# Performance work log

Measured on AMD Instinct MI355X. Metric: run time of the kernel, lower is better.

Reference implementation:

```python
import math
import jax, jax.numpy as jnp
import numpy as np

B, S, HID, NH = 8, 512, 1024, 16
D = HID // NH          # head dim = 64
SPAN = 512             # att_span = max_relative_positions = max_position_embeddings


def _linear(x, W, b):
    # torch nn.Linear: y = x @ W.T + b, W is [out, in]
    return jnp.einsum('...i,oi->...o', x, W) + b


def _heads(x):
    # [B, S, HID] -> [B, NH, S, D]
    b, s, _ = x.shape
    return x.reshape(b, s, NH, D).transpose(0, 2, 1, 3)


def setup_inputs() -> dict:
    key = jax.random.key(0)
    ks = jax.random.split(key, 16)
    f = lambda i, shape, sc=1.0: jax.random.normal(ks[i], shape, dtype=jnp.float32) * sc
    return {
        'q': f(0, (B, S, HID)),
        'k': f(1, (B, S, HID)),
        'v': f(2, (B, S, HID)),
        'attention_mask': jnp.tril(jnp.ones((S, S), dtype=bool))[None, None],  # causal [1,1,S,S]
        'Wq': f(3, (HID, HID), 0.02), 'bq': jnp.zeros((HID,), jnp.float32),
        'Wk': f(4, (HID, HID), 0.02), 'bk': jnp.zeros((HID,), jnp.float32),
        'Wv': f(5, (HID, HID), 0.02), 'bv': jnp.zeros((HID,), jnp.float32),
        'Wpk': f(6, (HID, HID), 0.02), 'bpk': jnp.zeros((HID,), jnp.float32),
        'Wpq': f(7, (HID, HID), 0.02), 'bpq': jnp.zeros((HID,), jnp.float32),
        'rel_emb': f(8, (2 * SPAN, HID), 0.02),
    }


def reference(q, k, v, attention_mask, Wq, bq, Wk, bk, Wv, bv, Wpk, bpk, Wpq, bpq, rel_emb):
    scale_factor = 3  # 1 (content) + c2p + p2c
    scale = 1.0 / math.sqrt(D * scale_factor)

    ql = _heads(_linear(q, Wq, bq))   # [B,NH,S,D]
    kl = _heads(_linear(k, Wk, bk))
    vl = _heads(_linear(v, Wv, bv))

    # content-to-content scores
    scores = jnp.einsum('bhqd,bhkd->bhqk', ql, kl) * scale

    # relative positions (no bucketing since position_buckets = -1)
    rel = jnp.arange(S)[:, None] - jnp.arange(S)[None, :]          # [S,S]
    c2p_pos = jnp.clip(rel + SPAN, 0, 2 * SPAN - 1)
    p2c_pos = jnp.clip(-rel + SPAN, 0, 2 * SPAN - 1)

    # projected relative-position embeddings -> [NH, 2*SPAN, D]
    pk = _linear(rel_emb, Wpk, bpk).reshape(2 * SPAN, NH, D).transpose(1, 0, 2)
    pq = _linear(rel_emb, Wpq, bpq).reshape(2 * SPAN, NH, D).transpose(1, 0, 2)

    # content-to-position: out[b,h,q,k] = (q . pos_key)[b,h,q, c2p_pos[q,k]]
    c2p = jnp.einsum('bhqd,hjd->bhqj', ql, pk) * scale             # [B,NH,S,2*SPAN]
    c2p = jnp.take_along_axis(c2p, jnp.broadcast_to(c2p_pos[None, None], (B, NH, S, S)), axis=-1)

    # position-to-content: gathered[b,h,k,q] = (k . pos_query)[b,h,k, p2c_pos[k,q]], then transpose
    p2c = jnp.einsum('bhkd,hjd->bhkj', kl, pq) * scale             # [B,NH,S,2*SPAN]
    p2c = jnp.take_along_axis(p2c, jnp.broadcast_to(p2c_pos[None, None], (B, NH, S, S)), axis=-1)

    scores = scores + c2p + jnp.swapaxes(p2c, -1, -2)
    # subtract detached row max (as in torch: .max(...).values.detach())
    scores = scores - jax.lax.stop_gradient(scores.max(axis=-1, keepdims=True))

    # XSoftmax: masked softmax, then zero masked positions
    neg = jnp.float32(-1e30)
    probs = jax.nn.softmax(jnp.where(attention_mask, scores, neg), axis=-1)
    probs = jnp.where(attention_mask, probs, 0.0)

    ctx = jnp.einsum('bhqk,bhkd->bhqd', probs, vl)                 # [B,NH,S,D]
    return ctx.transpose(0, 2, 1, 3).reshape(B, S, HID)
```

## Files before the change

kernel.cpp:

```cpp
#include <hip/hip_runtime.h>
#include <hip/hip_bf16.h>
#include <math.h>

#define SCALE 0.07216878364870323f
#define NEG_BIG -1e30f

typedef __attribute__((ext_vector_type(8))) short bf16x8;
typedef __attribute__((ext_vector_type(4))) short bf16x4;
typedef __attribute__((ext_vector_type(4))) float f32x4;
#define MFMA_BF16 __builtin_amdgcn_mfma_f32_16x16x32_bf16

#define BARX()   asm volatile("s_barrier" ::: "memory")
#define VMCNT0() asm volatile("s_waitcnt vmcnt(0)" ::: "memory")
#define LGKM0()  do { asm volatile("s_waitcnt lgkmcnt(0)" ::: "memory"); \
                      __builtin_amdgcn_sched_barrier(0); } while (0)

static __device__ __forceinline__ float bf2f(__hip_bfloat16 x) { return __bfloat162float(x); }
static __device__ __forceinline__ __hip_bfloat16 f2bf(float x) { return __float2bfloat16(x); }
static __device__ __forceinline__ short f2bs(float x) {
  union { __hip_bfloat16 b; short s; } u; u.b = __float2bfloat16(x); return u.s;
}
static __device__ __forceinline__ float s2f(short v) {
  union { float f; unsigned u; } x; x.u = ((unsigned)(unsigned short)v) << 16; return x.f;
}
static __device__ __forceinline__ bf16x4 cvt4(float4 f) {
  bf16x4 r; r[0] = f2bs(f.x); r[1] = f2bs(f.y); r[2] = f2bs(f.z); r[3] = f2bs(f.w);
  return r;
}
static __device__ __forceinline__ bf16x8 ldg8(const __hip_bfloat16* p) {
  return *(const bf16x8*)p;
}
static __device__ __forceinline__ void gl_lds16(const __hip_bfloat16* g, __hip_bfloat16* l) {
  __builtin_amdgcn_global_load_lds(
      (const __attribute__((address_space(1))) void*)g,
      (__attribute__((address_space(3))) void*)l, 16, 0, 0);
}

struct CvtJob { const float* src; __hip_bfloat16* dst; int n4; };
struct CvtArgs { CvtJob j[9]; };

__global__ __launch_bounds__(256) void cvt_kernel(CvtArgs a) {
  const CvtJob jb = a.j[blockIdx.y];
  const float4* s = (const float4*)jb.src;
  bf16x4* d = (bf16x4*)jb.dst;
  const int stride = gridDim.x * 256;
  for (int i = blockIdx.x * 256 + threadIdx.x; i < jb.n4; i += stride)
    d[i] = cvt4(s[i]);
}

struct Gemm { const __hip_bfloat16* A; const __hip_bfloat16* W;
              const float* bias; __hip_bfloat16* out; int mode; int mBits; int nBlk;
              float oscale; };
struct ProjArgs { Gemm g[5]; };

static __device__ __forceinline__ void stage_half(const __hip_bfloat16* gtile,
                                                  __hip_bfloat16* ltile,
                                                  int half, int wave, int lane) {
  const int r = lane >> 3;
  const int chunk = (lane & 7) ^ r;
#pragma unroll
  for (int c = 0; c < 2; c++) {
    const int rowbase = half * 128 + c * 64 + wave * 8;
    gl_lds16(gtile + (size_t)(rowbase + r) * 1024 + chunk * 8,
             ltile + (size_t)rowbase * 64);
  }
}

__global__ __launch_bounds__(512, 2) void proj_kernel(ProjArgs pa) {
  const Gemm g = pa.g[blockIdx.y];
  if ((int)blockIdx.x >= g.nBlk) return;
  __shared__ __hip_bfloat16 As[2][256][64];
  __shared__ __hip_bfloat16 Ws[2][256][64];

  const int bid = blockIdx.x;
  const int m0 = (bid & ((1 << g.mBits) - 1)) * 256;
  const int n0 = (bid >> g.mBits) * 256;
  const int tid = threadIdx.x;
  const int wave = tid >> 6, lane = tid & 63;
  const int q16 = lane >> 4, l16 = lane & 15;
  const int wr = wave >> 2, wc = wave & 3;
  const int l7 = l16 & 7;

  const __hip_bfloat16* Ag = g.A + (size_t)m0 * 1024;
  const __hip_bfloat16* Wg = g.W + (size_t)n0 * 1024;

  f32x4 acc[8][4] = {};

  stage_half(Ag, &As[0][0][0], 0, wave, lane);
  stage_half(Ag, &As[0][0][0], 1, wave, lane);
  stage_half(Wg, &Ws[0][0][0], 0, wave, lane);
  stage_half(Wg, &Ws[0][0][0], 1, wave, lane);
  VMCNT0();
  BARX();

  for (int t = 0; t < 16; ++t) {
    const int sl = t & 1, sn = sl ^ 1;
    const __hip_bfloat16* Ac = &As[sl][0][0];
    const __hip_bfloat16* Wc = &Ws[sl][0][0];
    const bool pf = (t + 1 < 16);
    const __hip_bfloat16* gA1 = Ag + (size_t)(t + 1) * 64;
    const __hip_bfloat16* gW1 = Wg + (size_t)(t + 1) * 64;

    bf16x8 bw[4], af[4];
#pragma unroll
    for (int kh = 0; kh < 2; kh++) {
      const int csw = ((kh * 4 + q16) ^ l7) * 8;

#pragma unroll
      for (int ni = 0; ni < 4; ni++)
        bw[ni] = *(const bf16x8*)(Wc + (size_t)(wc * 64 + ni * 16 + l16) * 64 + csw);
#pragma unroll
      for (int mi = 0; mi < 4; mi++)
        af[mi] = *(const bf16x8*)(Ac + (size_t)(wr * 128 + mi * 16 + l16) * 64 + csw);
      if (pf) {
        if (kh == 0) stage_half(gA1, &As[sn][0][0], 0, wave, lane);
        else         stage_half(gW1, &Ws[sn][0][0], 0, wave, lane);
      }
      BARX();
      LGKM0();
      __builtin_amdgcn_s_setprio(1);
#pragma unroll
      for (int ni = 0; ni < 4; ni++)
#pragma unroll
        for (int mi = 0; mi < 4; mi++)
          acc[mi][ni] = MFMA_BF16(af[mi], bw[ni], acc[mi][ni], 0, 0, 0);
      __builtin_amdgcn_s_setprio(0);
      BARX();

#pragma unroll
      for (int mi = 0; mi < 4; mi++)
        af[mi] = *(const bf16x8*)(Ac + (size_t)(wr * 128 + 64 + mi * 16 + l16) * 64 + csw);
      if (pf) {
        if (kh == 0) stage_half(gA1, &As[sn][0][0], 1, wave, lane);
        else         stage_half(gW1, &Ws[sn][0][0], 1, wave, lane);
      }
      BARX();
      LGKM0();
      __builtin_amdgcn_s_setprio(1);
#pragma unroll
      for (int ni = 0; ni < 4; ni++)
#pragma unroll
        for (int mi = 0; mi < 4; mi++)
          acc[4 + mi][ni] = MFMA_BF16(af[mi], bw[ni], acc[4 + mi][ni], 0, 0, 0);
      __builtin_amdgcn_s_setprio(0);
      if (kh == 1 && pf) VMCNT0();
      BARX();
    }
  }

#pragma unroll
  for (int ni = 0; ni < 4; ni++) {
    const int n = n0 + wc * 64 + ni * 16 + l16;
#pragma unroll
    for (int mi = 0; mi < 8; mi++) {
#pragma unroll
      for (int rr = 0; rr < 4; rr++) {
        const int m = m0 + wr * 128 + mi * 16 + q16 * 4 + rr;
        float val = acc[mi][ni][rr];
        size_t oidx;
        if (g.mode == 0) {
          val = (val + g.bias[n]) * g.oscale;
          const int b = m >> 9, s = m & 511;
          const int h = n >> 6, d = n & 63;
          oidx = ((size_t)((b * 16 + h) * 512 + s)) * 64 + d;
        } else if (g.mode == 1) {
          val = (val + g.bias[m]) * g.oscale;
          const int b = n >> 9, s = n & 511;
          const int h = m >> 6, d = m & 63;
          oidx = ((size_t)((b * 16 + h) * 64 + d)) * 512 + s;
        } else {
          val = (val + g.bias[n]) * g.oscale;
          const int h = n >> 6, d = n & 63;
          oidx = ((size_t)(h * 512 + m)) * 64 + d;
        }
        g.out[oidx] = f2bf(val);
      }
    }
  }
}

__global__ __launch_bounds__(256) void attn_kernel(
    const __hip_bfloat16* __restrict__ ql,
    const __hip_bfloat16* __restrict__ kl,
    const __hip_bfloat16* __restrict__ vlT,
    const __hip_bfloat16* __restrict__ pk,
    const __hip_bfloat16* __restrict__ pq,
    float* __restrict__ out)
{
  __shared__ __align__(16) __hip_bfloat16 pool[2][64][72];
  __shared__ __align__(16) __hip_bfloat16 pqs[2][32][72];
  __shared__ __align__(16) float qkbuf[32][36];
  __shared__ __align__(16) __hip_bfloat16 cpb[2][32][68];
  __shared__ __align__(16) __hip_bfloat16 pT[64][36];
  __shared__ __align__(16) __hip_bfloat16 ptile[32][40];
  __shared__ __align__(16) __hip_bfloat16 vt[64][40];
  __shared__ float mred[32];
  __shared__ float rsum[32];

  const int bid = blockIdx.x;
  const int qt = 15 - (bid >> 7);
  const int bh = bid & 127;
  const int h = bh & 15, b = bh >> 4;
  const int q0 = qt * 32;

  const __hip_bfloat16* qlp = ql + (size_t)bh * 512 * 64;
  const __hip_bfloat16* klp = kl + (size_t)bh * 512 * 64;
  const __hip_bfloat16* vtp = vlT + (size_t)bh * 64 * 512;
  const __hip_bfloat16* pkp = pk + (size_t)h * 512 * 64;
  const __hip_bfloat16* pqp = pq + (size_t)h * 512 * 64;

  const int tid = threadIdx.x, wave = tid >> 6, lane = tid & 63;
  const int q16 = lane >> 4, l16 = lane & 15;
  const int wr = wave & 1, wc = wave >> 1;

  bf16x8 qlB[2][2];
#pragma unroll
  for (int ksi = 0; ksi < 2; ksi++)
#pragma unroll
    for (int bq = 0; bq < 2; bq++)
      qlB[ksi][bq] = ldg8(qlp + (size_t)(q0 + bq * 16 + l16) * 64 + ksi * 32 + q16 * 8);

  {
    int4 z = {0, 0, 0, 0};
    *(int4*)(&pqs[1][tid >> 3][(tid & 7) * 8]) = z;
  }

  const int kEnd = q0 + 32;
  const int nIter = kEnd >> 5;

  const int sr = tid >> 3, sseg = tid & 7;
  const int vr = tid >> 2, vs = tid & 3;
  int4 rKv, rPKv, rPQv, rVt;
  {
    rKv  = ((const int4*)(klp + (size_t)(q0 + sr) * 64))[sseg];
    rPKv = ((const int4*)(pkp + (size_t)(0 + sr) * 64))[sseg];
    rPQv = ((const int4*)(pqp + (size_t)(0 + sr) * 64))[sseg];
    rVt  = ((const int4*)(vtp + (size_t)vr * 512 + q0))[vs];
  }

  const int aq = tid >> 3;
  const int kb = (tid & 7) * 4;
  float m_old = -INFINITY, s_part = 0.f;
  f32x4 octx[2] = {};

  for (int it = 0; it < nIter; ++it) {
    const int k0 = q0 - it * 32;
    const int par = it & 1;
    *(int4*)(&pool[par][sr][sseg * 8])      = rKv;
    *(int4*)(&pool[par][32 + sr][sseg * 8]) = rPKv;
    *(int4*)(&pqs[par][sr][sseg * 8])       = rPQv;
    if (it + 1 < nIter) {
      const int k0n = k0 - 32, jbn = (it + 1) * 32;
      rKv  = ((const int4*)(klp + (size_t)(k0n + sr) * 64))[sseg];
      rPKv = ((const int4*)(pkp + (size_t)(jbn + sr) * 64))[sseg];
      rPQv = ((const int4*)(pqp + (size_t)(jbn + sr) * 64))[sseg];
    }
    __syncthreads();

    const int arb = (wave == 1) ? 32 : 0;
    f32x4 a4[2][2] = {};
    __builtin_amdgcn_s_setprio(1);
#pragma unroll
    for (int ksi = 0; ksi < 2; ksi++) {
      const int ko = ksi * 32 + q16 * 8;
      bf16x8 Af0 = *(const bf16x8*)(&pool[par][arb + l16][ko]);
      bf16x8 Af1 = *(const bf16x8*)(&pool[par][arb + 16 + l16][ko]);
      bf16x8 Bf0, Bf1;
      if (wave < 2) {
        Bf0 = qlB[ksi][0];
        Bf1 = qlB[ksi][1];
      } else {
        const int ps = (wave == 2) ? (par ^ 1) : par;
        Bf0 = *(const bf16x8*)(&pqs[ps][l16][ko]);
        Bf1 = *(const bf16x8*)(&pqs[ps][16 + l16][ko]);
      }
      a4[0][0] = MFMA_BF16(Af0, Bf0, a4[0][0], 0, 0, 0);
      a4[0][1] = MFMA_BF16(Af0, Bf1, a4[0][1], 0, 0, 0);
      a4[1][0] = MFMA_BF16(Af1, Bf0, a4[1][0], 0, 0, 0);
      a4[1][1] = MFMA_BF16(Af1, Bf1, a4[1][1], 0, 0, 0);
    }
    __builtin_amdgcn_s_setprio(0);
    if (wave == 0) {
#pragma unroll
      for (int a = 0; a < 2; a++)
#pragma unroll
        for (int bq = 0; bq < 2; bq++)
          *(f32x4*)(&qkbuf[bq * 16 + l16][a * 16 + q16 * 4]) = a4[a][bq];
    } else if (wave == 1) {
#pragma unroll
      for (int a = 0; a < 2; a++)
#pragma unroll
        for (int bq = 0; bq < 2; bq++) {
          bf16x4 v;
#pragma unroll
          for (int r = 0; r < 4; r++) v[r] = f2bs(a4[a][bq][r]);
          const int q = bq * 16 + l16, jr = a * 16 + q16 * 4;
          *(bf16x4*)(&cpb[par][q][32 + jr]) = v;
          *(bf16x4*)(&cpb[par ^ 1][q][jr]) = v;
        }
    } else {
      const int rb = (wave == 3) ? 32 : 0;
#pragma unroll
      for (int a = 0; a < 2; a++)
#pragma unroll
        for (int bq = 0; bq < 2; bq++) {
          bf16x4 v;
#pragma unroll
          for (int r = 0; r < 4; r++) v[r] = f2bs(a4[a][bq][r]);
          *(bf16x4*)(&pT[rb + bq * 16 + l16][a * 16 + q16 * 4]) = v;
        }
    }
    __syncthreads();

    {
      const f32x4 qk4 = *(const f32x4*)(&qkbuf[aq][kb]);
      float v[4];
      float tmax = -INFINITY;
#pragma unroll
      for (int j = 0; j < 4; j++) {
        const int dlt = aq - (kb + j);
        v[j] = qk4[j] + bf2f(cpb[par][aq][dlt + 32]) + bf2f(pT[dlt + 32][kb + j]);
        if ((it == 0) && (dlt < 0)) v[j] = -INFINITY;
        else tmax = fmaxf(tmax, v[j]);
      }
      tmax = fmaxf(tmax, __shfl_xor(tmax, 1));
      tmax = fmaxf(tmax, __shfl_xor(tmax, 2));
      tmax = fmaxf(tmax, __shfl_xor(tmax, 4));
      const float m_new = fmaxf(m_old, tmax);
      const float f = __expf(m_old - m_new);
      bf16x4 pv4;
      float psum = 0.f;
#pragma unroll
      for (int j = 0; j < 4; j++) {
        const float p = __expf(v[j] - m_new);
        pv4[j] = f2bs(p);
        psum += p;
      }
      s_part = s_part * f + psum;
      m_old = m_new;
      *(bf16x4*)(&ptile[aq][kb]) = pv4;
      if ((tid & 7) == 0) mred[aq] = f;
    }
    {
      *(int4*)(&vt[vr][vs * 8]) = rVt;
      if (it + 1 < nIter)
        rVt = ((const int4*)(vtp + (size_t)vr * 512 + (k0 - 32)))[vs];
    }
    __syncthreads();

    {
      float fr[4];
#pragma unroll
      for (int rr = 0; rr < 4; rr++) fr[rr] = mred[wr * 16 + q16 * 4 + rr];
      bf16x8 af = *(const bf16x8*)(&ptile[wr * 16 + l16][q16 * 8]);
      __builtin_amdgcn_s_setprio(1);
#pragma unroll
      for (int cs = 0; cs < 2; cs++) {
        bf16x8 bv = *(const bf16x8*)(&vt[wc * 32 + cs * 16 + l16][q16 * 8]);
        f32x4 c = octx[cs];
#pragma unroll
        for (int rr = 0; rr < 4; rr++) c[rr] *= fr[rr];
        octx[cs] = MFMA_BF16(af, bv, c, 0, 0, 0);
      }
      __builtin_amdgcn_s_setprio(0);
    }
  }

  {
    float s = s_part;
    s += __shfl_xor(s, 1);
    s += __shfl_xor(s, 2);
    s += __shfl_xor(s, 4);
    if ((tid & 7) == 0) rsum[aq] = s;
  }
  __syncthreads();

  for (int cs = 0; cs < 2; cs++) {
    const int d = wc * 32 + cs * 16 + l16;
    for (int rr = 0; rr < 4; rr++) {
      const int qh = wr * 16 + q16 * 4 + rr;
      const float val = octx[cs][rr] / rsum[qh];
      out[((size_t)(b * 512 + q0 + qh)) * 1024 + h * 64 + d] = val;
    }
  }
}

extern "C" void kernel_launch(void* const* d_in, const int* in_sizes, int n_in,
                              void* d_out, int out_size, void* d_ws, size_t ws_size,
                              hipStream_t stream) {
  const float* q   = (const float*)d_in[0];
  const float* k   = (const float*)d_in[1];
  const float* v   = (const float*)d_in[2];
  const float* Wq  = (const float*)d_in[4];
  const float* bq  = (const float*)d_in[5];
  const float* Wk  = (const float*)d_in[6];
  const float* bk  = (const float*)d_in[7];
  const float* Wv  = (const float*)d_in[8];
  const float* bv  = (const float*)d_in[9];
  const float* Wpk = (const float*)d_in[10];
  const float* bpk = (const float*)d_in[11];
  const float* Wpq = (const float*)d_in[12];
  const float* bpq = (const float*)d_in[13];
  const float* rel = (const float*)d_in[14];
  float* out = (float*)d_out;

  char* ws = (char*)d_ws;
  const size_t MB = 1u << 20;
  __hip_bfloat16* bqi  = (__hip_bfloat16*)(ws);
  __hip_bfloat16* bki  = (__hip_bfloat16*)(ws + 8 * MB);
  __hip_bfloat16* bvi  = (__hip_bfloat16*)(ws + 16 * MB);
  __hip_bfloat16* bWq  = (__hip_bfloat16*)(ws + 24 * MB);
  __hip_bfloat16* bWk  = (__hip_bfloat16*)(ws + 26 * MB);
  __hip_bfloat16* bWv  = (__hip_bfloat16*)(ws + 28 * MB);
  __hip_bfloat16* bWpk = (__hip_bfloat16*)(ws + 30 * MB);
  __hip_bfloat16* bWpq = (__hip_bfloat16*)(ws + 32 * MB);
  __hip_bfloat16* brel = (__hip_bfloat16*)(ws + 34 * MB);
  __hip_bfloat16* wql  = (__hip_bfloat16*)(ws + 35 * MB);
  __hip_bfloat16* wkl  = (__hip_bfloat16*)(ws + 43 * MB);
  __hip_bfloat16* wvlT = (__hip_bfloat16*)(ws + 51 * MB);
  __hip_bfloat16* wpk  = (__hip_bfloat16*)(ws + 59 * MB);
  __hip_bfloat16* wpq  = (__hip_bfloat16*)(ws + 60 * MB);

  CvtArgs ca;
  ca.j[0] = { q,   bqi,  4194304 / 4 };
  ca.j[1] = { k,   bki,  4194304 / 4 };
  ca.j[2] = { v,   bvi,  4194304 / 4 };
  ca.j[3] = { Wq,  bWq,  1048576 / 4 };
  ca.j[4] = { Wk,  bWk,  1048576 / 4 };
  ca.j[5] = { Wv,  bWv,  1048576 / 4 };
  ca.j[6] = { Wpk, bWpk, 1048576 / 4 };
  ca.j[7] = { Wpq, bWpq, 1048576 / 4 };
  ca.j[8] = { rel + (size_t)512 * 1024, brel, 524288 / 4 };
  cvt_kernel<<<dim3(1024, 9), 256, 0, stream>>>(ca);

  ProjArgs pj;
  pj.g[0] = { bqi,  bWq,  bq,  wql,  0, 4, 64, SCALE };
  pj.g[1] = { bki,  bWk,  bk,  wkl,  0, 4, 64, 1.0f };
  pj.g[2] = { bWv,  bvi,  bv,  wvlT, 1, 2, 64, 1.0f };
  pj.g[3] = { brel, bWpk, bpk, wpk,  2, 1, 8,  1.0f };
  pj.g[4] = { brel, bWpq, bpq, wpq,  2, 1, 8,  SCALE };
  proj_kernel<<<dim3(64, 5), 512, 0, stream>>>(pj);

  attn_kernel<<<2048, 256, 0, stream>>>(wql, wkl, wvlT, wpk, wpq, out);
}
```

Baseline: 231.4 us.

## Shrink projection GEMM tile to 256x128 and drop double-buffered LDS pipeline

```diff
diff --git a/kernel.cpp b/kernel.cpp
--- a/kernel.cpp
+++ b/kernel.cpp
@@ -9,11 +9,6 @@
 typedef __attribute__((ext_vector_type(4))) short bf16x4;
 typedef __attribute__((ext_vector_type(4))) float f32x4;
 #define MFMA_BF16 __builtin_amdgcn_mfma_f32_16x16x32_bf16
-
-#define BARX()   asm volatile("s_barrier" ::: "memory")
-#define VMCNT0() asm volatile("s_waitcnt vmcnt(0)" ::: "memory")
-#define LGKM0()  do { asm volatile("s_waitcnt lgkmcnt(0)" ::: "memory"); \
-                      __builtin_amdgcn_sched_barrier(0); } while (0)
 
 static __device__ __forceinline__ float bf2f(__hip_bfloat16 x) { return __bfloat162float(x); }
 static __device__ __forceinline__ __hip_bfloat16 f2bf(float x) { return __float2bfloat16(x); }
@@ -53,14 +48,15 @@
               float oscale; };
 struct ProjArgs { Gemm g[5]; };
 
-static __device__ __forceinline__ void stage_half(const __hip_bfloat16* gtile,
+static __device__ __forceinline__ void stage_tile(const __hip_bfloat16* gtile,
                                                   __hip_bfloat16* ltile,
-                                                  int half, int wave, int lane) {
+                                                  int nrows, int wave, int lane) {
   const int r = lane >> 3;
   const int chunk = (lane & 7) ^ r;
 #pragma unroll
-  for (int c = 0; c < 2; c++) {
-    const int rowbase = half * 128 + c * 64 + wave * 8;
+  for (int c = 0; c < 4; c++) {
+    if (c * 64 >= nrows) break;
+    const int rowbase = c * 64 + wave * 8;
     gl_lds16(gtile + (size_t)(rowbase + r) * 1024 + chunk * 8,
              ltile + (size_t)rowbase * 64);
   }
@@ -69,55 +65,38 @@
 __global__ __launch_bounds__(512, 2) void proj_kernel(ProjArgs pa) {
   const Gemm g = pa.g[blockIdx.y];
   if ((int)blockIdx.x >= g.nBlk) return;
-  __shared__ __hip_bfloat16 As[2][256][64];
-  __shared__ __hip_bfloat16 Ws[2][256][64];
+  __shared__ __hip_bfloat16 As[256][64];
+  __shared__ __hip_bfloat16 Ws[128][64];
 
   const int bid = blockIdx.x;
   const int m0 = (bid & ((1 << g.mBits) - 1)) * 256;
-  const int n0 = (bid >> g.mBits) * 256;
+  const int n0 = (bid >> g.mBits) * 128;
   const int tid = threadIdx.x;
   const int wave = tid >> 6, lane = tid & 63;
   const int q16 = lane >> 4, l16 = lane & 15;
-  const int wr = wave >> 2, wc = wave & 3;
+  const int wr = wave >> 1, wc = wave & 1;
   const int l7 = l16 & 7;
 
   const __hip_bfloat16* Ag = g.A + (size_t)m0 * 1024;
   const __hip_bfloat16* Wg = g.W + (size_t)n0 * 1024;
 
-  f32x4 acc[8][4] = {};
-
-  stage_half(Ag, &As[0][0][0], 0, wave, lane);
-  stage_half(Ag, &As[0][0][0], 1, wave, lane);
-  stage_half(Wg, &Ws[0][0][0], 0, wave, lane);
-  stage_half(Wg, &Ws[0][0][0], 1, wave, lane);
-  VMCNT0();
-  BARX();
+  f32x4 acc[4][4] = {};
 
   for (int t = 0; t < 16; ++t) {
-    const int sl = t & 1, sn = sl ^ 1;
-    const __hip_bfloat16* Ac = &As[sl][0][0];
-    const __hip_bfloat16* Wc = &Ws[sl][0][0];
-    const bool pf = (t + 1 < 16);
-    const __hip_bfloat16* gA1 = Ag + (size_t)(t + 1) * 64;
-    const __hip_bfloat16* gW1 = Wg + (size_t)(t + 1) * 64;
-
-    bf16x8 bw[4], af[4];
+    __syncthreads();
+    stage_tile(Ag + t * 64, &As[0][0], 256, wave, lane);
+    stage_tile(Wg + t * 64, &Ws[0][0], 128, wave, lane);
+    __syncthreads();
 #pragma unroll
     for (int kh = 0; kh < 2; kh++) {
       const int csw = ((kh * 4 + q16) ^ l7) * 8;
-
+      bf16x8 bw[4], af[4];
 #pragma unroll
       for (int ni = 0; ni < 4; ni++)
-        bw[ni] = *(const bf16x8*)(Wc + (size_t)(wc * 64 + ni * 16 + l16) * 64 + csw);
+        bw[ni] = *(const bf16x8*)(&Ws[wc * 64 + ni * 16 + l16][0] + csw);
 #pragma unroll
       for (int mi = 0; mi < 4; mi++)
-        af[mi] = *(const bf16x8*)(Ac + (size_t)(wr * 128 + mi * 16 + l16) * 64 + csw);
-      if (pf) {
-        if (kh == 0) stage_half(gA1, &As[sn][0][0], 0, wave, lane);
-        else         stage_half(gW1, &Ws[sn][0][0], 0, wave, lane);
-      }
-      BARX();
-      LGKM0();
+        af[mi] = *(const bf16x8*)(&As[wr * 64 + mi * 16 + l16][0] + csw);
       __builtin_amdgcn_s_setprio(1);
 #pragma unroll
       for (int ni = 0; ni < 4; ni++)
@@ -125,26 +104,6 @@
         for (int mi = 0; mi < 4; mi++)
           acc[mi][ni] = MFMA_BF16(af[mi], bw[ni], acc[mi][ni], 0, 0, 0);
       __builtin_amdgcn_s_setprio(0);
-      BARX();
-
-#pragma unroll
-      for (int mi = 0; mi < 4; mi++)
-        af[mi] = *(const bf16x8*)(Ac + (size_t)(wr * 128 + 64 + mi * 16 + l16) * 64 + csw);
-      if (pf) {
-        if (kh == 0) stage_half(gA1, &As[sn][0][0], 1, wave, lane);
-        else         stage_half(gW1, &Ws[sn][0][0], 1, wave, lane);
-      }
-      BARX();
-      LGKM0();
-      __builtin_amdgcn_s_setprio(1);
-#pragma unroll
-      for (int ni = 0; ni < 4; ni++)
-#pragma unroll
-        for (int mi = 0; mi < 4; mi++)
-          acc[4 + mi][ni] = MFMA_BF16(af[mi], bw[ni], acc[4 + mi][ni], 0, 0, 0);
-      __builtin_amdgcn_s_setprio(0);
-      if (kh == 1 && pf) VMCNT0();
-      BARX();
     }
   }
 
@@ -152,10 +111,10 @@
   for (int ni = 0; ni < 4; ni++) {
     const int n = n0 + wc * 64 + ni * 16 + l16;
 #pragma unroll
-    for (int mi = 0; mi < 8; mi++) {
+    for (int mi = 0; mi < 4; mi++) {
 #pragma unroll
       for (int rr = 0; rr < 4; rr++) {
-        const int m = m0 + wr * 128 + mi * 16 + q16 * 4 + rr;
+        const int m = m0 + wr * 64 + mi * 16 + q16 * 4 + rr;
         float val = acc[mi][ni][rr];
         size_t oidx;
         if (g.mode == 0) {
@@ -434,12 +393,12 @@
   cvt_kernel<<<dim3(1024, 9), 256, 0, stream>>>(ca);
 
   ProjArgs pj;
-  pj.g[0] = { bqi,  bWq,  bq,  wql,  0, 4, 64, SCALE };
-  pj.g[1] = { bki,  bWk,  bk,  wkl,  0, 4, 64, 1.0f };
-  pj.g[2] = { bWv,  bvi,  bv,  wvlT, 1, 2, 64, 1.0f };
-  pj.g[3] = { brel, bWpk, bpk, wpk,  2, 1, 8,  1.0f };
-  pj.g[4] = { brel, bWpq, bpq, wpq,  2, 1, 8,  SCALE };
-  proj_kernel<<<dim3(64, 5), 512, 0, stream>>>(pj);
+  pj.g[0] = { bqi,  bWq,  bq,  wql,  0, 4, 128, SCALE };
+  pj.g[1] = { bki,  bWk,  bk,  wkl,  0, 4, 128, 1.0f };
+  pj.g[2] = { bWv,  bvi,  bv,  wvlT, 1, 2, 128, 1.0f };
+  pj.g[3] = { brel, bWpk, bpk, wpk,  2, 1, 16,  1.0f };
+  pj.g[4] = { brel, bWpq, bpq, wpq,  2, 1, 16,  SCALE };
+  proj_kernel<<<dim3(128, 5), 512, 0, stream>>>(pj);
 
   attn_kernel<<<2048, 256, 0, stream>>>(wql, wkl, wvlT, wpk, wpq, out);
 }
```

Result: faster. 222.8 us (-3.7%).
